# Kernel optimization log

Measured on AMD Instinct MI355X. Metric: run time of the kernel, lower is better.

## Reference

```python
import jax, jax.numpy as jnp
import numpy as np

OVERSAMP = 2


def _pad_last2(x, H2, W2):
    # centered zero-pad of last two dims to (H2, W2) -- PadLast
    H, W = x.shape[-2], x.shape[-1]
    ph, pw = (H2 - H) // 2, (W2 - W) // 2
    pad = [(0, 0)] * (x.ndim - 2) + [(ph, H2 - H - ph), (pw, W2 - W - pw)]
    return jnp.pad(x, pad)


def _crop_last2(x, H, W):
    # centered crop of last two dims to (H, W) -- PadLast.adjoint
    H2, W2 = x.shape[-2], x.shape[-1]
    ph, pw = (H2 - H) // 2, (W2 - W) // 2
    return x[..., ph:ph + H, pw:pw + W]


def setup_inputs() -> dict:
    key = jax.random.key(0)
    ks = jax.random.split(key, 6)
    A, C, H, W = 5, 12, 256, 256
    Hp, Wp = OVERSAMP * H, OVERSAMP * W
    x_r = jax.random.normal(ks[0], (A, H, W), dtype=jnp.float32)
    x_i = jax.random.normal(ks[1], (A, H, W), dtype=jnp.float32)
    mps_r = jax.random.normal(ks[2], (C, H, W), dtype=jnp.float32) * 0.1
    mps_i = jax.random.normal(ks[3], (C, H, W), dtype=jnp.float32) * 0.1
    kern_r = jax.random.normal(ks[4], (A, A, Hp, Wp), dtype=jnp.float32) * 0.1
    kern_i = jax.random.normal(ks[5], (A, A, Hp, Wp), dtype=jnp.float32) * 0.1
    return {"x_r": x_r, "x_i": x_i, "mps_r": mps_r, "mps_i": mps_i,
            "kern_r": kern_r, "kern_i": kern_i}


def reference(x_r, x_i, mps_r, mps_i, kern_r, kern_i):
    # Toeplitz normal operator AHA_func: x [A,H,W] -> [A,H,W]
    x = jax.lax.complex(x_r, x_i)          # [A,H,W]
    mps = jax.lax.complex(mps_r, mps_i)    # [C,H,W]
    kernels = jax.lax.complex(kern_r, kern_i)  # [Aout,Ain,2H,2W]
    A, H, W = x.shape
    Hp, Wp = kernels.shape[-2], kernels.shape[-1]
    # coil modulation: x[None,:] * mps[:,None] -> [C,A,H,W]
    cx = mps[:, None, :, :] * x[None, :, :, :]
    cx = _pad_last2(cx, Hp, Wp)            # [C,A,2H,2W]
    Fx = jnp.fft.fftn(cx, axes=(-2, -1), norm='ortho')
    # Fx[:,None] [C,1,Ain,2H,2W] * kernels [Aout,Ain,2H,2W] -> [C,Aout,Ain,2H,2W]
    y = (OVERSAMP ** 2) * jnp.fft.ifftn(Fx[:, None, ...] * kernels,
                                        axes=(-2, -1), norm='ortho')
    y = jnp.sum(y, axis=2)                 # sum over Ain -> [C,Aout,2H,2W]
    y = _crop_last2(y, H, W)               # [C,A,H,W]
    y = y * jnp.conj(mps)[:, None, :, :]
    return jnp.sum(y, axis=0)              # [A,H,W]
```

## Files before the change

### kernel.cpp

```cpp
#include <hip/hip_runtime.h>
#include <cstddef>

#define A_  5
#define C_  12
#define RPG (C_ * A_)
#define TWO_PI 6.28318530717958647692f
#define NPAD 596

__device__ float2 g_bufA[RPG * 512 * 256];
__device__ float2 g_bufB[RPG * 512 * 256];

__device__ __forceinline__ int P5(int i) { return i + 5 * (i >> 5); }
__device__ __forceinline__ int PT(int i) { return i + (i >> 3); }

__device__ __forceinline__ void build_tab256(float2* tab, int t) {
    if (t < 256) {
        float s, c;
        __sincosf(-TWO_PI * (float)t * (1.0f / 512.0f), &s, &c);
        tab[PT(t)] = make_float2(c, s);
    }
}

template<int DIR>
__device__ __forceinline__ float2 cmulw(float2 v, float2 w) {
    float cv = w.x, sv = (DIR < 0) ? w.y : -w.y;
    return make_float2(v.x * cv - v.y * sv, v.x * sv + v.y * cv);
}

template<int DIR>
__device__ __forceinline__ void dft8(float* xr, float* xi) {
    const float S = 0.70710678118654752f;
    float ar[4], ai[4], br[4], bi[4];
#pragma unroll
    for (int j = 0; j < 4; ++j) {
        ar[j] = xr[j] + xr[j+4]; ai[j] = xi[j] + xi[j+4];
        br[j] = xr[j] - xr[j+4]; bi[j] = xi[j] - xi[j+4];
    }
    float t;
    if (DIR < 0) {
        t = S*(br[1]+bi[1]); bi[1] = S*(bi[1]-br[1]); br[1] = t;
        t = bi[2];           bi[2] = -br[2];          br[2] = t;
        t = S*(bi[3]-br[3]); bi[3] = -S*(br[3]+bi[3]); br[3] = t;
    } else {
        t = S*(br[1]-bi[1]); bi[1] = S*(bi[1]+br[1]); br[1] = t;
        t = -bi[2];          bi[2] = br[2];           br[2] = t;
        t = -S*(br[3]+bi[3]); bi[3] = S*(br[3]-bi[3]); br[3] = t;
    }
    float c0r=ar[0]+ar[2], c0i=ai[0]+ai[2], c1r=ar[1]+ar[3], c1i=ai[1]+ai[3];
    float d0r=ar[0]-ar[2], d0i=ai[0]-ai[2], d1r, d1i;
    if (DIR < 0) { d1r =  ai[1]-ai[3]; d1i = -(ar[1]-ar[3]); }
    else         { d1r = -(ai[1]-ai[3]); d1i =  ar[1]-ar[3]; }
    xr[0]=c0r+c1r; xi[0]=c0i+c1i; xr[4]=c0r-c1r; xi[4]=c0i-c1i;
    xr[2]=d0r+d1r; xi[2]=d0i+d1i; xr[6]=d0r-d1r; xi[6]=d0i-d1i;
    c0r=br[0]+br[2]; c0i=bi[0]+bi[2]; c1r=br[1]+br[3]; c1i=bi[1]+bi[3];
    d0r=br[0]-br[2]; d0i=bi[0]-bi[2];
    if (DIR < 0) { d1r =  bi[1]-bi[3]; d1i = -(br[1]-br[3]); }
    else         { d1r = -(bi[1]-bi[3]); d1i =  br[1]-br[3]; }
    xr[1]=c0r+c1r; xi[1]=c0i+c1i; xr[5]=c0r-c1r; xi[5]=c0i-c1i;
    xr[3]=d0r+d1r; xi[3]=d0i+d1i; xr[7]=d0r-d1r; xi[7]=d0i-d1i;
}

__device__ __forceinline__ void twiddle_chain(float* vr, float* vi, float ang) {
    float s, c; __sincosf(ang, &s, &c);
    float twr = c, twi = s;
#pragma unroll
    for (int d = 1; d < 8; ++d) {
        float tr = vr[d]*twr - vi[d]*twi;
        vi[d]    = vr[d]*twi + vi[d]*twr;
        vr[d]    = tr;
        float nr = twr*c - twi*s;
        twi      = twr*s + twi*c;
        twr      = nr;
    }
}

template<int DIR>
__device__ __forceinline__ void wfft512(float* vr, float* vi,
                                        float* sre, float* sim, int lh) {
    const float sgn = (DIR < 0) ? -1.f : 1.f;
    dft8<DIR>(vr, vi);
    twiddle_chain(vr, vi, sgn * (TWO_PI/512.f) * (float)lh);
#pragma unroll
    for (int d = 0; d < 8; ++d) { sre[72*d+lh] = vr[d]; sim[72*d+lh] = vi[d]; }
    asm volatile("s_waitcnt lgkmcnt(0)" ::: "memory");
    int rb = 72*(lh>>3) + (lh&7);
#pragma unroll
    for (int e = 0; e < 8; ++e) { vr[e] = sre[rb+8*e]; vi[e] = sim[rb+8*e]; }
    dft8<DIR>(vr, vi);
    twiddle_chain(vr, vi, sgn * (TWO_PI/64.f) * (float)(lh & 7));
    int wb = 9*(lh>>3) + (lh&7);
#pragma unroll
    for (int h = 0; h < 8; ++h) { sre[72*h+wb] = vr[h]; sim[72*h+wb] = vi[h]; }
    asm volatile("s_waitcnt lgkmcnt(0)" ::: "memory");
    int rb2 = 72*(lh&7) + 9*(lh>>3);
#pragma unroll
    for (int f = 0; f < 8; ++f) { vr[f] = sre[rb2+f]; vi[f] = sim[rb2+f]; }
    dft8<DIR>(vr, vi);
}

template<int DIR>
__device__ void fftB4(float (*AR)[NPAD], float (*AI)[NPAD],
                      float (*BR)[NPAD], float (*BI)[NPAD],
                      const float2* tab, int t) {
    int tt = t & 127, b0 = (t >> 7) << 1;
    float (*sR)[NPAD] = AR; float (*sI)[NPAD] = AI;
    float (*dR)[NPAD] = BR; float (*dI)[NPAD] = BI;
    int Ns = 1;
    #pragma unroll
    for (int s = 0; s < 4; ++s) {
        __syncthreads();
        int m = tt & (Ns - 1);
        int e1 = m << (7 - 2 * s);
        float2 w1 = tab[PT(e1)], w2 = tab[PT(2 * e1)];
        float2 w3 = make_float2(w1.x * w2.x - w1.y * w2.y,
                                w1.x * w2.y + w1.y * w2.x);
        int i0 = P5(tt), i1 = P5(tt + 128), i2 = P5(tt + 256), i3 = P5(tt + 384);
        int idxD = ((tt & ~(Ns - 1)) << 2) | m;
        int o0 = P5(idxD), o1 = P5(idxD + Ns);
        int o2 = P5(idxD + 2 * Ns), o3 = P5(idxD + 3 * Ns);
        #pragma unroll
        for (int bb = 0; bb < 2; ++bb) {
            int b = b0 + bb;
            float2 v0 = make_float2(sR[b][i0], sI[b][i0]);
            float2 v1 = cmulw<DIR>(make_float2(sR[b][i1], sI[b][i1]), w1);
            float2 v2 = cmulw<DIR>(make_float2(sR[b][i2], sI[b][i2]), w2);
            float2 v3 = cmulw<DIR>(make_float2(sR[b][i3], sI[b][i3]), w3);
            float2 t0 = make_float2(v0.x + v2.x, v0.y + v2.y);
            float2 t1 = make_float2(v0.x - v2.x, v0.y - v2.y);
            float2 t2 = make_float2(v1.x + v3.x, v1.y + v3.y);
            float2 t3 = make_float2(v1.x - v3.x, v1.y - v3.y);
            float2 y0 = make_float2(t0.x + t2.x, t0.y + t2.y);
            float2 y2 = make_float2(t0.x - t2.x, t0.y - t2.y);
            float2 y1, y3;
            if (DIR < 0) {
                y1 = make_float2(t1.x + t3.y, t1.y - t3.x);
                y3 = make_float2(t1.x - t3.y, t1.y + t3.x);
            } else {
                y1 = make_float2(t1.x - t3.y, t1.y + t3.x);
                y3 = make_float2(t1.x + t3.y, t1.y - t3.x);
            }
            dR[b][o0] = y0.x; dI[b][o0] = y0.y;
            dR[b][o1] = y1.x; dI[b][o1] = y1.y;
            dR[b][o2] = y2.x; dI[b][o2] = y2.y;
            dR[b][o3] = y3.x; dI[b][o3] = y3.y;
        }
        { auto tp = sR; sR = dR; dR = tp; }
        { auto tp = sI; sI = dI; dI = tp; }
        Ns <<= 2;
    }
    __syncthreads();
    #pragma unroll
    for (int q = 0; q < 2; ++q) {
        int j2 = tt + q * 128;
        float2 w = tab[PT(j2)];
        int i0 = P5(j2), i1 = P5(j2 + 256);
        #pragma unroll
        for (int bb = 0; bb < 2; ++bb) {
            int b = b0 + bb;
            float2 v0 = make_float2(sR[b][i0], sI[b][i0]);
            float2 tw = cmulw<DIR>(make_float2(sR[b][i1], sI[b][i1]), w);
            dR[b][i0] = v0.x + tw.x; dI[b][i0] = v0.y + tw.y;
            dR[b][i1] = v0.x - tw.x; dI[b][i1] = v0.y - tw.y;
        }
    }
    __syncthreads();
}

__global__ void k_zero(float* __restrict__ out, int n) {
    int i = blockIdx.x * 256 + threadIdx.x;
    int stride = gridDim.x * 256;
    for (; i < n; i += stride) out[i] = 0.f;
}

__global__ void __launch_bounds__(256) k_fft1c(const float* __restrict__ xr_,
        const float* __restrict__ xi_, const float* __restrict__ mr_,
        const float* __restrict__ mi_) {
    __shared__ float AR[4][NPAD], AI[4][NPAD], BR[4][NPAD], BI[4][NPAD];
    __shared__ float2 tab[288];
    int bid = blockIdx.x;
    int ca = bid >> 6;
    int x0 = (bid & 63) << 2;
    int coil = ca / A_, a = ca % A_;
    int t = threadIdx.x;
    build_tab256(tab, t);
    int xc = t & 3, yo = t >> 2;
    int xcol = x0 + xc;
    const float* xr = xr_ + a * 65536;
    const float* xi = xi_ + a * 65536;
    const float* mr = mr_ + coil * 65536;
    const float* mi = mi_ + coil * 65536;
    #pragma unroll
    for (int r = 0; r < 2; ++r) {
        int z = yo + 64 * r;
        AR[xc][P5(z)] = 0.f;        AI[xc][P5(z)] = 0.f;
        AR[xc][P5(384 + z)] = 0.f;  AI[xc][P5(384 + z)] = 0.f;
    }
    #pragma unroll
    for (int r = 0; r < 4; ++r) {
        int y = yo + 64 * r;
        int idx = y * 256 + xcol;
        float xrv = xr[idx], xiv = xi[idx], mrv = mr[idx], miv = mi[idx];
        int p = P5(128 + y);
        AR[xc][p] = xrv * mrv - xiv * miv;
        AI[xc][p] = xrv * miv + xiv * mrv;
    }
    fftB4<-1>(AR, AI, BR, BI, tab, t);
    float2* o = g_bufA + (size_t)ca * 131072 + x0 + xc;
    #pragma unroll
    for (int rr = 0; rr < 8; ++rr) {
        int ky = yo + 64 * rr;
        int p = P5(ky);
        o[(size_t)ky * 256] = make_float2(BR[xc][p], BI[xc][p]);
    }
}

__global__ void __launch_bounds__(320) k_colfmc(const float* __restrict__ kr,
                                                const float* __restrict__ ki) {
    __shared__ float FRe[A_][512], FIm[A_][512];
    __shared__ float shR[A_][576], shI[A_][576];
    int b = blockIdx.x;
    int xcd = b & 7, s = b >> 3;
    int v = s / 96, wv = s % 96;
    int u = xcd + (v << 3);
    int coil = wv % C_;
    int ky = (u << 3) + (wv / C_);
    int t = threadIdx.x;
    int w = t >> 6, L = t & 63;
    int sig = ((L & 7) << 3) | (L >> 3);
    float* sre = shR[w]; float* sim = shI[w];

    {
        const float2* row = g_bufA + (size_t)(coil * A_ + w) * 131072 +
                            ((size_t)ky << 8);
        float vr[8], vi[8];
        #pragma unroll
        for (int r = 0; r < 8; ++r) { vr[r] = 0.f; vi[r] = 0.f; }
        #pragma unroll
        for (int r = 2; r < 6; ++r) {
            float2 vv = row[((r - 2) << 6) + L];
            vr[r] = vv.x; vi[r] = vv.y;
        }
        wfft512<-1>(vr, vi, sre, sim, L);
        #pragma unroll
        for (int g = 0; g < 8; ++g) {
            int kx = (g << 6) + sig;
            FRe[w][kx] = vr[g]; FIm[w][kx] = vi[g];
        }
    }
    __syncthreads();

    const float scale = 4.0f / 262144.0f;
    if (t < 256) {
        size_t kyb = (size_t)ky << 9;
        #pragma unroll
        for (int h = 0; h < 2; ++h) {
            int kx = t + (h << 8);
            float fr[A_], fi[A_];
            #pragma unroll
            for (int ain = 0; ain < A_; ++ain) {
                fr[ain] = FRe[ain][kx]; fi[ain] = FIm[ain][kx];
            }
            float gr[A_], gi[A_];
            #pragma unroll
            for (int ao = 0; ao < A_; ++ao) {
                float ar = 0.f, ai = 0.f;
                #pragma unroll
                for (int ain = 0; ain < A_; ++ain) {
                    size_t idx = ((size_t)(ao * A_ + ain) << 18) + kyb + kx;
                    float kre = kr[idx], kim = ki[idx];
                    ar += kre * fr[ain] - kim * fi[ain];
                    ai += kre * fi[ain] + kim * fr[ain];
                }
                gr[ao] = scale * ar; gi[ao] = scale * ai;
            }
            #pragma unroll
            for (int ao = 0; ao < A_; ++ao) {
                FRe[ao][kx] = gr[ao]; FIm[ao][kx] = gi[ao];
            }
        }
    }
    __syncthreads();

    {
        float vr[8], vi[8];
        #pragma unroll
        for (int r = 0; r < 8; ++r) {
            int kx = (r << 6) + sig;
            vr[r] = FRe[w][kx]; vi[r] = FIm[w][kx];
        }
        wfft512<1>(vr, vi, sre, sim, sig);
        float2* oB = g_bufB + (size_t)(coil * A_ + w) * 131072 +
                     ((size_t)ky << 8);
        #pragma unroll
        for (int g = 2; g < 6; ++g)
            oB[((g - 2) << 6) + L] = make_float2(vr[g], vi[g]);
    }
}

__global__ void __launch_bounds__(256) k_outfr(const float* __restrict__ mr_,
        const float* __restrict__ mi_, float* __restrict__ out, int outFloats) {
    __shared__ float AR[4][NPAD], AI[4][NPAD], BR[4][NPAD], BI[4][NPAD];
    __shared__ float2 tab[288];
    int bid = blockIdx.x;
    int a = bid >> 8;
    int x0 = ((bid >> 2) & 63) << 2;
    int cg = bid & 3;
    int t = threadIdx.x;
    build_tab256(tab, t);
    int xc = t & 3, yo = t >> 2;
    int xcol = x0 + xc;
    float accR[4], accI[4];
    #pragma unroll
    for (int r = 0; r < 4; ++r) { accR[r] = 0.f; accI[r] = 0.f; }
    for (int cc = 0; cc < 3; ++cc) {
        int c = cg * 3 + cc;
        const float2* src = g_bufB + (size_t)(c * A_ + a) * 131072 + xcol;
        #pragma unroll
        for (int rr = 0; rr < 8; ++rr) {
            int ky = yo + 64 * rr;
            float2 vv = src[(size_t)ky * 256];
            int p = P5(ky);
            AR[xc][p] = vv.x; AI[xc][p] = vv.y;
        }
        fftB4<1>(AR, AI, BR, BI, tab, t);
        const float* mr = mr_ + c * 65536;
        const float* mi = mi_ + c * 65536;
        #pragma unroll
        for (int rr = 0; rr < 4; ++rr) {
            int y = yo + 64 * rr;
            int p = P5(128 + y);
            float vx = BR[xc][p], vy = BI[xc][p];
            int idx = y * 256 + xcol;
            float mrv = mr[idx], miv = mi[idx];
            accR[rr] += vx * mrv + vy * miv;
            accI[rr] += vy * mrv - vx * miv;
        }
    }
    #pragma unroll
    for (int rr = 0; rr < 4; ++rr) {
        int y = yo + 64 * rr;
        size_t r0 = (size_t)a * 65536 + (size_t)y * 256 + xcol;
        size_t i0 = 327680 + r0;
        if (r0 < (size_t)outFloats) atomicAdd(&out[r0], accR[rr]);
        if (i0 < (size_t)outFloats) atomicAdd(&out[i0], accI[rr]);
    }
}

extern "C" void kernel_launch(void* const* d_in, const int* in_sizes, int n_in,
                              void* d_out, int out_size, void* d_ws, size_t ws_size,
                              hipStream_t stream) {
    const float* xr = (const float*)d_in[0];
    const float* xi = (const float*)d_in[1];
    const float* mr = (const float*)d_in[2];
    const float* mi = (const float*)d_in[3];
    const float* kr = (const float*)d_in[4];
    const float* ki = (const float*)d_in[5];
    float* out = (float*)d_out;
    (void)d_ws; (void)ws_size; (void)n_in; (void)in_sizes;

    int nz = out_size < 655360 ? out_size : 655360;
    k_zero  <<<256, 256, 0, stream>>>(out, nz);
    k_fft1c <<<RPG * 64, 256, 0, stream>>>(xr, xi, mr, mi);
    k_colfmc<<<C_ * 512, 320, 0, stream>>>(kr, ki);
    k_outfr <<<A_ * 256, 256, 0, stream>>>(mr, mi, out, out_size);
}
```

Measured before the change: 350.8 us.

## Reuse kernel values in registers across three coils per block in colfmc

The middle kernel now keeps all 25 kernel-matrix entries for one kx column in registers and loops over three coils per block, where before it re-read them from global memory for every coil. The grid moves to 2048 blocks of 512 threads: 5 warps run the row FFTs and all 512 threads do the per-frequency 5x5 mixing. The column-FFT kernels drop to 128 threads per block, each thread now doing the full butterfly work for 4 columns. The aim is to cut kernel-tensor traffic about 12x-to-4x, at the cost of higher register pressure, extra barriers and idle warps during the FFT phases.

```diff
diff --git a/kernel.cpp b/kernel.cpp
--- a/kernel.cpp
+++ b/kernel.cpp
@@ -13,11 +13,13 @@
 __device__ __forceinline__ int P5(int i) { return i + 5 * (i >> 5); }
 __device__ __forceinline__ int PT(int i) { return i + (i >> 3); }
 
-__device__ __forceinline__ void build_tab256(float2* tab, int t) {
-    if (t < 256) {
+__device__ __forceinline__ void build_tab(float2* tab, int t) {
+    #pragma unroll
+    for (int q = 0; q < 2; ++q) {
+        int k = t + q * 128;
         float s, c;
-        __sincosf(-TWO_PI * (float)t * (1.0f / 512.0f), &s, &c);
-        tab[PT(t)] = make_float2(c, s);
+        __sincosf(-TWO_PI * (float)k * (1.0f / 512.0f), &s, &c);
+        tab[PT(k)] = make_float2(c, s);
     }
 }
 
@@ -98,29 +100,27 @@
     dft8<DIR>(vr, vi);
 }
 
-template<int DIR>
-__device__ void fftB4(float (*AR)[NPAD], float (*AI)[NPAD],
-                      float (*BR)[NPAD], float (*BI)[NPAD],
-                      const float2* tab, int t) {
-    int tt = t & 127, b0 = (t >> 7) << 1;
+template<int DIR, int NB>
+__device__ void fftB(float (*AR)[NPAD], float (*AI)[NPAD],
+                     float (*BR)[NPAD], float (*BI)[NPAD],
+                     const float2* tab, int t) {
     float (*sR)[NPAD] = AR; float (*sI)[NPAD] = AI;
     float (*dR)[NPAD] = BR; float (*dI)[NPAD] = BI;
     int Ns = 1;
     #pragma unroll
     for (int s = 0; s < 4; ++s) {
         __syncthreads();
-        int m = tt & (Ns - 1);
+        int m = t & (Ns - 1);
         int e1 = m << (7 - 2 * s);
         float2 w1 = tab[PT(e1)], w2 = tab[PT(2 * e1)];
         float2 w3 = make_float2(w1.x * w2.x - w1.y * w2.y,
                                 w1.x * w2.y + w1.y * w2.x);
-        int i0 = P5(tt), i1 = P5(tt + 128), i2 = P5(tt + 256), i3 = P5(tt + 384);
-        int idxD = ((tt & ~(Ns - 1)) << 2) | m;
+        int i0 = P5(t), i1 = P5(t + 128), i2 = P5(t + 256), i3 = P5(t + 384);
+        int idxD = ((t & ~(Ns - 1)) << 2) | m;
         int o0 = P5(idxD), o1 = P5(idxD + Ns);
         int o2 = P5(idxD + 2 * Ns), o3 = P5(idxD + 3 * Ns);
         #pragma unroll
-        for (int bb = 0; bb < 2; ++bb) {
-            int b = b0 + bb;
+        for (int b = 0; b < NB; ++b) {
             float2 v0 = make_float2(sR[b][i0], sI[b][i0]);
             float2 v1 = cmulw<DIR>(make_float2(sR[b][i1], sI[b][i1]), w1);
             float2 v2 = cmulw<DIR>(make_float2(sR[b][i2], sI[b][i2]), w2);
@@ -151,12 +151,11 @@
     __syncthreads();
     #pragma unroll
     for (int q = 0; q < 2; ++q) {
-        int j2 = tt + q * 128;
+        int j2 = t + q * 128;
         float2 w = tab[PT(j2)];
         int i0 = P5(j2), i1 = P5(j2 + 256);
         #pragma unroll
-        for (int bb = 0; bb < 2; ++bb) {
-            int b = b0 + bb;
+        for (int b = 0; b < NB; ++b) {
             float2 v0 = make_float2(sR[b][i0], sI[b][i0]);
             float2 tw = cmulw<DIR>(make_float2(sR[b][i1], sI[b][i1]), w);
             dR[b][i0] = v0.x + tw.x; dI[b][i0] = v0.y + tw.y;
@@ -172,7 +171,7 @@
     for (; i < n; i += stride) out[i] = 0.f;
 }
 
-__global__ void __launch_bounds__(256) k_fft1c(const float* __restrict__ xr_,
+__global__ void __launch_bounds__(128) k_fft1c(const float* __restrict__ xr_,
         const float* __restrict__ xi_, const float* __restrict__ mr_,
         const float* __restrict__ mi_) {
     __shared__ float AR[4][NPAD], AI[4][NPAD], BR[4][NPAD], BI[4][NPAD];
@@ -182,7 +181,7 @@
     int x0 = (bid & 63) << 2;
     int coil = ca / A_, a = ca % A_;
     int t = threadIdx.x;
-    build_tab256(tab, t);
+    build_tab(tab, t);
     int xc = t & 3, yo = t >> 2;
     int xcol = x0 + xc;
     const float* xr = xr_ + a * 65536;
@@ -190,75 +189,81 @@
     const float* mr = mr_ + coil * 65536;
     const float* mi = mi_ + coil * 65536;
     #pragma unroll
-    for (int r = 0; r < 2; ++r) {
-        int z = yo + 64 * r;
+    for (int r = 0; r < 4; ++r) {
+        int z = yo + 32 * r;
         AR[xc][P5(z)] = 0.f;        AI[xc][P5(z)] = 0.f;
         AR[xc][P5(384 + z)] = 0.f;  AI[xc][P5(384 + z)] = 0.f;
     }
     #pragma unroll
-    for (int r = 0; r < 4; ++r) {
-        int y = yo + 64 * r;
+    for (int r = 0; r < 8; ++r) {
+        int y = yo + 32 * r;
         int idx = y * 256 + xcol;
         float xrv = xr[idx], xiv = xi[idx], mrv = mr[idx], miv = mi[idx];
         int p = P5(128 + y);
         AR[xc][p] = xrv * mrv - xiv * miv;
         AI[xc][p] = xrv * miv + xiv * mrv;
     }
-    fftB4<-1>(AR, AI, BR, BI, tab, t);
+    fftB<-1, 4>(AR, AI, BR, BI, tab, t);
     float2* o = g_bufA + (size_t)ca * 131072 + x0 + xc;
     #pragma unroll
-    for (int rr = 0; rr < 8; ++rr) {
-        int ky = yo + 64 * rr;
+    for (int rr = 0; rr < 16; ++rr) {
+        int ky = yo + 32 * rr;
         int p = P5(ky);
         o[(size_t)ky * 256] = make_float2(BR[xc][p], BI[xc][p]);
     }
 }
 
-__global__ void __launch_bounds__(320) k_colfmc(const float* __restrict__ kr,
-                                                const float* __restrict__ ki) {
+__global__ void __launch_bounds__(512, 4) k_colfmc(const float* __restrict__ kr,
+                                                   const float* __restrict__ ki) {
     __shared__ float FRe[A_][512], FIm[A_][512];
     __shared__ float shR[A_][576], shI[A_][576];
     int b = blockIdx.x;
     int xcd = b & 7, s = b >> 3;
-    int v = s / 96, wv = s % 96;
-    int u = xcd + (v << 3);
-    int coil = wv % C_;
-    int ky = (u << 3) + (wv / C_);
+    int ky = (xcd << 6) + (s >> 2);
+    int tc = s & 3;
     int t = threadIdx.x;
     int w = t >> 6, L = t & 63;
     int sig = ((L & 7) << 3) | (L >> 3);
-    float* sre = shR[w]; float* sim = shI[w];
-
+
+    float kR[25], kI[25];
     {
-        const float2* row = g_bufA + (size_t)(coil * A_ + w) * 131072 +
-                            ((size_t)ky << 8);
-        float vr[8], vi[8];
-        #pragma unroll
-        for (int r = 0; r < 8; ++r) { vr[r] = 0.f; vi[r] = 0.f; }
-        #pragma unroll
-        for (int r = 2; r < 6; ++r) {
-            float2 vv = row[((r - 2) << 6) + L];
-            vr[r] = vv.x; vi[r] = vv.y;
-        }
-        wfft512<-1>(vr, vi, sre, sim, L);
-        #pragma unroll
-        for (int g = 0; g < 8; ++g) {
-            int kx = (g << 6) + sig;
-            FRe[w][kx] = vr[g]; FIm[w][kx] = vi[g];
-        }
-    }
-    __syncthreads();
-
+        size_t kb = ((size_t)ky << 9) + t;
+        #pragma unroll
+        for (int m = 0; m < 25; ++m) {
+            kR[m] = kr[((size_t)m << 18) + kb];
+            kI[m] = ki[((size_t)m << 18) + kb];
+        }
+    }
     const float scale = 4.0f / 262144.0f;
-    if (t < 256) {
-        size_t kyb = (size_t)ky << 9;
-        #pragma unroll
-        for (int h = 0; h < 2; ++h) {
-            int kx = t + (h << 8);
+
+    for (int cc = 0; cc < 3; ++cc) {
+        int coil = tc * 3 + cc;
+
+        if (w < A_) {
+            const float2* row = g_bufA + (size_t)(coil * A_ + w) * 131072 +
+                                ((size_t)ky << 8);
+            float vr[8], vi[8];
+            #pragma unroll
+            for (int r = 0; r < 8; ++r) { vr[r] = 0.f; vi[r] = 0.f; }
+            #pragma unroll
+            for (int r = 2; r < 6; ++r) {
+                float2 vv = row[((r - 2) << 6) + L];
+                vr[r] = vv.x; vi[r] = vv.y;
+            }
+            wfft512<-1>(vr, vi, shR[w], shI[w], L);
+            #pragma unroll
+            for (int g = 0; g < 8; ++g) {
+                int kx = (g << 6) + sig;
+                FRe[w][kx] = vr[g]; FIm[w][kx] = vi[g];
+            }
+        }
+        __syncthreads();
+
+        {
             float fr[A_], fi[A_];
             #pragma unroll
             for (int ain = 0; ain < A_; ++ain) {
-                fr[ain] = FRe[ain][kx]; fi[ain] = FIm[ain][kx];
+                fr[ain] = FRe[ain][t]; fi[ain] = FIm[ain][t];
             }
             float gr[A_], gi[A_];
             #pragma unroll
@@ -266,8 +271,7 @@
                 float ar = 0.f, ai = 0.f;
                 #pragma unroll
                 for (int ain = 0; ain < A_; ++ain) {
-                    size_t idx = ((size_t)(ao * A_ + ain) << 18) + kyb + kx;
-                    float kre = kr[idx], kim = ki[idx];
+                    float kre = kR[ao * A_ + ain], kim = kI[ao * A_ + ain];
                     ar += kre * fr[ain] - kim * fi[ain];
                     ai += kre * fi[ain] + kim * fr[ain];
                 }
@@ -275,29 +279,30 @@
             }
             #pragma unroll
             for (int ao = 0; ao < A_; ++ao) {
-                FRe[ao][kx] = gr[ao]; FIm[ao][kx] = gi[ao];
-            }
-        }
-    }
-    __syncthreads();
-
-    {
-        float vr[8], vi[8];
-        #pragma unroll
-        for (int r = 0; r < 8; ++r) {
-            int kx = (r << 6) + sig;
-            vr[r] = FRe[w][kx]; vi[r] = FIm[w][kx];
-        }
-        wfft512<1>(vr, vi, sre, sim, sig);
-        float2* oB = g_bufB + (size_t)(coil * A_ + w) * 131072 +
-                     ((size_t)ky << 8);
-        #pragma unroll
-        for (int g = 2; g < 6; ++g)
-            oB[((g - 2) << 6) + L] = make_float2(vr[g], vi[g]);
-    }
-}
-
-__global__ void __launch_bounds__(256) k_outfr(const float* __restrict__ mr_,
+                FRe[ao][t] = gr[ao]; FIm[ao][t] = gi[ao];
+            }
+        }
+        __syncthreads();
+
+        if (w < A_) {
+            float vr[8], vi[8];
+            #pragma unroll
+            for (int r = 0; r < 8; ++r) {
+                int kx = (r << 6) + sig;
+                vr[r] = FRe[w][kx]; vi[r] = FIm[w][kx];
+            }
+            wfft512<1>(vr, vi, shR[w], shI[w], sig);
+            float2* oB = g_bufB + (size_t)(coil * A_ + w) * 131072 +
+                         ((size_t)ky << 8);
+            #pragma unroll
+            for (int g = 2; g < 6; ++g)
+                oB[((g - 2) << 6) + L] = make_float2(vr[g], vi[g]);
+        }
+        __syncthreads();
+    }
+}
+
+__global__ void __launch_bounds__(128) k_outfr(const float* __restrict__ mr_,
         const float* __restrict__ mi_, float* __restrict__ out, int outFloats) {
     __shared__ float AR[4][NPAD], AI[4][NPAD], BR[4][NPAD], BI[4][NPAD];
     __shared__ float2 tab[288];
@@ -306,28 +311,28 @@
     int x0 = ((bid >> 2) & 63) << 2;
     int cg = bid & 3;
     int t = threadIdx.x;
-    build_tab256(tab, t);
+    build_tab(tab, t);
     int xc = t & 3, yo = t >> 2;
     int xcol = x0 + xc;
-    float accR[4], accI[4];
-    #pragma unroll
-    for (int r = 0; r < 4; ++r) { accR[r] = 0.f; accI[r] = 0.f; }
+    float accR[8], accI[8];
+    #pragma unroll
+    for (int r = 0; r < 8; ++r) { accR[r] = 0.f; accI[r] = 0.f; }
     for (int cc = 0; cc < 3; ++cc) {
         int c = cg * 3 + cc;
         const float2* src = g_bufB + (size_t)(c * A_ + a) * 131072 + xcol;
         #pragma unroll
-        for (int rr = 0; rr < 8; ++rr) {
-            int ky = yo + 64 * rr;
+        for (int rr = 0; rr < 16; ++rr) {
+            int ky = yo + 32 * rr;
             float2 vv = src[(size_t)ky * 256];
             int p = P5(ky);
             AR[xc][p] = vv.x; AI[xc][p] = vv.y;
         }
-        fftB4<1>(AR, AI, BR, BI, tab, t);
+        fftB<1, 4>(AR, AI, BR, BI, tab, t);
         const float* mr = mr_ + c * 65536;
         const float* mi = mi_ + c * 65536;
         #pragma unroll
-        for (int rr = 0; rr < 4; ++rr) {
-            int y = yo + 64 * rr;
+        for (int rr = 0; rr < 8; ++rr) {
+            int y = yo + 32 * rr;
             int p = P5(128 + y);
             float vx = BR[xc][p], vy = BI[xc][p];
             int idx = y * 256 + xcol;
@@ -337,8 +342,8 @@
         }
     }
     #pragma unroll
-    for (int rr = 0; rr < 4; ++rr) {
-        int y = yo + 64 * rr;
+    for (int rr = 0; rr < 8; ++rr) {
+        int y = yo + 32 * rr;
         size_t r0 = (size_t)a * 65536 + (size_t)y * 256 + xcol;
         size_t i0 = 327680 + r0;
         if (r0 < (size_t)outFloats) atomicAdd(&out[r0], accR[rr]);
@@ -360,7 +365,7 @@
 
     int nz = out_size < 655360 ? out_size : 655360;
     k_zero  <<<256, 256, 0, stream>>>(out, nz);
-    k_fft1c <<<RPG * 64, 256, 0, stream>>>(xr, xi, mr, mi);
-    k_colfmc<<<C_ * 512, 320, 0, stream>>>(kr, ki);
-    k_outfr <<<A_ * 256, 256, 0, stream>>>(mr, mi, out, out_size);
-}
+    k_fft1c <<<RPG * 64, 128, 0, stream>>>(xr, xi, mr, mi);
+    k_colfmc<<<2048, 512, 0, stream>>>(kr, ki);
+    k_outfr <<<A_ * 256, 128, 0, stream>>>(mr, mi, out, out_size);
+}
```

After: 373.9 us. +6.6%, slower.
